# Kernel tuning notes

Hardware: AMD Instinct MI355X
Metric: run time of the kernel (lower is better)

The kernel has to match this reference:

```python
import jax, jax.numpy as jnp
import numpy as np

N_FFT = 4096
HOP = 1024
MAX_FRAMES = 345  # 44100*8 // 1024 + 1
BATCH = 8


def _build_buffers():
    N = N_FFT
    half = N // 2
    n = np.arange(N)
    k = np.arange(half + 1)
    ang = 2.0 * np.pi * np.outer(k, n) / N
    # fourier_basis = [real(fft(eye)[:half+1]); imag(fft(eye)[:half+1])], W[k,n]=exp(-2pi i kn/N)
    F = np.vstack([np.cos(ang), -np.sin(ang)])  # [N+2, N], float64
    window = 0.5 - 0.5 * np.cos(2.0 * np.pi * n / N)  # periodic hann, max == 1.0
    # rows of F are mutually orthogonal -> pinv(F) = F.T @ diag(1/||row||^2) (zero rows -> 0)
    norms = np.sum(F ** 2, axis=1)
    inv_norm = np.where(norms > 1e-6, 1.0 / norms, 0.0)
    # inverse_basis = window * pinv(F * N/HOP).T * sqrt(N)   (normalized=True)
    scale = inv_norm * (HOP / N) * np.sqrt(N)
    inverse_basis = (window[None, :] * F * scale[:, None]).astype(np.float32)  # [N+2, N]
    # window_sum normalization buffer
    T = MAX_FRAMES
    n_len = N + HOP * (T - 1)
    win_sq = (window / np.abs(window).max()) ** 2
    window_sum = np.zeros(n_len, dtype=np.float64)
    for i in range(T):
        s = i * HOP
        window_sum[s:s + N] += win_sq
    window_sum_inv = (N / (window_sum * HOP + 1e-8)).astype(np.float32)  # [n_len]
    return jnp.asarray(inverse_basis), jnp.asarray(window_sum_inv)


def setup_inputs() -> dict:
    key = jax.random.key(0)
    k1, k2 = jax.random.split(key)
    real = jax.random.normal(k1, (BATCH, N_FFT // 2 + 1, MAX_FRAMES), dtype=jnp.float32)
    imag = jax.random.normal(k2, (BATCH, N_FFT // 2 + 1, MAX_FRAMES), dtype=jnp.float32)
    inverse_basis, window_sum_inv = _build_buffers()
    return {"real": real, "imag": imag, "inverse_basis": inverse_basis,
            "window_sum_inv": window_sum_inv, "length": 352800}


def reference(real, imag, inverse_basis, window_sum_inv, length):
    eps = jnp.finfo(real.dtype).eps
    magnitude = jnp.sqrt(real ** 2 + imag ** 2)
    phase = jnp.arctan2(imag, real + eps)
    # [B, N+2, T]
    complex_input = jnp.concatenate([magnitude * jnp.cos(phase),
                                     magnitude * jnp.sin(phase)], axis=1)
    # conv_transpose1d(stride=HOP) == per-frame IDFT matmul + overlap-add
    frames = jnp.einsum('bct,ck->btk', complex_input, inverse_basis)  # [B, T, N]
    B, T, K = frames.shape
    n_len = K + HOP * (T - 1)
    idx = (jnp.arange(T)[:, None] * HOP + jnp.arange(K)[None, :]).reshape(-1)
    sig = jnp.zeros((B, n_len), frames.dtype).at[:, idx].add(frames.reshape(B, -1))
    half = K // 2
    out = sig[:, half:] * window_sum_inv[half:n_len]  # [B, n_len - half]
    if length:
        pad = max(0, length - out.shape[-1])
        out = jnp.pad(out, ((0, 0), (0, pad)))[:, :length]
    return out
```

## Files before the change

### kernel.cpp

```cpp
#include <hip/hip_runtime.h>
#include <cstdint>
#include <cstddef>

#define B_SZ  8
#define C_IN  2049
#define T_FR  345
#define NFFT  4096
#define HOPSZ 1024
#define MFR   2760
#define NPAIR 173
#define TW    1.5339807878856412e-3f

typedef float f4 __attribute__((ext_vector_type(4)));

__device__ __forceinline__ unsigned short f2b(float f) {
  union { float f; unsigned int u; } v; v.f = f;
  unsigned int r = v.u + 0x7fffu + ((v.u >> 16) & 1u);
  return (unsigned short)(r >> 16);
}
__device__ __forceinline__ float b2f(unsigned int h) {
  union { unsigned int u; float f; } v; v.u = h << 16;
  return v.f;
}

__global__ void trans(const float* __restrict__ re, const float* __restrict__ im,
                      unsigned int* __restrict__ spec) {
  __shared__ float tr[64][65];
  __shared__ float ti[64][65];
  const int tid = threadIdx.x;
  const int t0 = blockIdx.x * 64;
  const int c0 = blockIdx.y * 64;
  const int b  = blockIdx.z;
#pragma unroll
  for (int pass = 0; pass < 16; ++pass) {
    int idx = pass * 256 + tid;
    int tt = idx & 63, cc = idx >> 6;
    int c = c0 + cc, t = t0 + tt;
    float rp = 0.f, ip = 0.f;
    if (c < C_IN && t < T_FR) {
      size_t off = ((size_t)b * C_IN + c) * T_FR + t;
      float r = re[off], i = im[off];
      float x  = r + 1.1920929e-7f;
      float r2 = r * r + i * i;
      float h2 = fmaxf(x * x + i * i, 1e-35f);
      float inv = __builtin_amdgcn_sqrtf(r2) * __builtin_amdgcn_rsqf(h2);
      rp = x * inv;
      ip = i * inv;
    }
    tr[cc][tt] = rp;
    ti[cc][tt] = ip;
  }
  __syncthreads();
#pragma unroll
  for (int pass = 0; pass < 16; ++pass) {
    int idx = pass * 256 + tid;
    int kk = idx & 63, tt = idx >> 6;
    int c = c0 + kk, t = t0 + tt;
    if (c < C_IN && t < T_FR) {
      size_t mrow = (size_t)b * T_FR + t;
      unsigned int pk = ((unsigned int)f2b(ti[kk][tt]) << 16) | f2b(tr[kk][tt]);
      spec[mrow * C_IN + c] = pk;
    }
  }
}

template<int M, int L2M>
__device__ __forceinline__ void fft_stage(const f4* __restrict__ sr, const f4* __restrict__ si,
                                          f4* __restrict__ dr, f4* __restrict__ di, int tid) {
  f4 ar = sr[tid],       ai = si[tid];
  f4 br = sr[tid + 256], bi = si[tid + 256];
  f4 cr = sr[tid + 512], ci = si[tid + 512];
  f4 er = sr[tid + 768], ei = si[tid + 768];
  f4 t0r = ar + cr, t0i = ai + ci;
  f4 t1r = ar - cr, t1i = ai - ci;
  f4 t2r = br + er, t2i = bi + ei;
  f4 t3r = ei - bi, t3i = br - er;
  f4 y0r = t0r + t2r, y0i = t0i + t2i;
  f4 u1r = t1r + t3r, u1i = t1i + t3i;
  f4 u2r = t0r - t2r, u2i = t0i - t2i;
  f4 u3r = t1r - t3r, u3i = t1i - t3i;
  const int base = tid << 2;
  if (M == 1) {
#pragma unroll
    for (int p = 0; p < 4; ++p) {
      int j = base + p;
      float s1, c1; __sincosf((float)j * TW, &s1, &c1);
      float c2 = c1 * c1 - s1 * s1, s2 = 2.f * c1 * s1;
      float c3 = c2 * c1 - s2 * s1, s3 = s2 * c1 + c2 * s1;
      f4 o, oi;
      o.x  = y0r[p];
      o.y  = c1 * u1r[p] - s1 * u1i[p];
      o.z  = c2 * u2r[p] - s2 * u2i[p];
      o.w  = c3 * u3r[p] - s3 * u3i[p];
      oi.x = y0i[p];
      oi.y = c1 * u1i[p] + s1 * u1r[p];
      oi.z = c2 * u2i[p] + s2 * u2r[p];
      oi.w = c3 * u3i[p] + s3 * u3r[p];
      dr[j] = o; di[j] = oi;
    }
  } else {
    const int j  = base >> L2M;
    const int kb = (base & (M - 1)) >> 2;
    float s1, c1; __sincosf((float)(j * M) * TW, &s1, &c1);
    float c2 = c1 * c1 - s1 * s1, s2 = 2.f * c1 * s1;
    float c3 = c2 * c1 - s2 * s1, s3 = s2 * c1 + c2 * s1;
    const int wb = kb + M * j;
    const int Q  = M >> 2;
    dr[wb]         = y0r;                      di[wb]         = y0i;
    dr[wb + Q]     = c1 * u1r - s1 * u1i;      di[wb + Q]     = c1 * u1i + s1 * u1r;
    dr[wb + 2 * Q] = c2 * u2r - s2 * u2i;      di[wb + 2 * Q] = c2 * u2i + s2 * u2r;
    dr[wb + 3 * Q] = c3 * u3r - s3 * u3i;      di[wb + 3 * Q] = c3 * u3i + s3 * u3r;
  }
}

__global__ __launch_bounds__(256) void ifft_frames(const unsigned int* __restrict__ spec,
                                                   unsigned short* __restrict__ Fr) {
  __shared__ f4 B0r[1024], B0i[1024], B1r[1024], B1i[1024];
  float* r0 = (float*)B0r;
  float* i0 = (float*)B0i;
  const int tid = threadIdx.x;
  const int j = blockIdx.x, b = blockIdx.y;
  const int ta = b * T_FR + 2 * j;
  const bool hasb = (2 * j + 1) < T_FR;
  const unsigned int* spa = spec + (size_t)ta * C_IN;
  const unsigned int* spb = spa + C_IN;
#pragma unroll
  for (int p = 0; p < 8; ++p) {
    int k = p * 256 + tid;
    unsigned int va = spa[k];
    unsigned int vb = hasb ? spb[k] : 0u;
    float ar = b2f(va & 0xffffu), ai = b2f(va >> 16);
    float br = b2f(vb & 0xffffu), bi = b2f(vb >> 16);
    if (k == 0) {
      r0[0] = ar; i0[0] = br;
    } else {
      r0[k] = ar - bi;        i0[k] = ai + br;
      r0[4096 - k] = ar + bi; i0[4096 - k] = br - ai;
    }
  }
  if (tid == 0) {
    unsigned int va = spa[2048];
    unsigned int vb = hasb ? spb[2048] : 0u;
    r0[2048] = b2f(va & 0xffffu);
    i0[2048] = b2f(vb & 0xffffu);
  }
  __syncthreads();
  fft_stage<1,    0>(B0r, B0i, B1r, B1i, tid); __syncthreads();
  fft_stage<4,    2>(B1r, B1i, B0r, B0i, tid); __syncthreads();
  fft_stage<16,   4>(B0r, B0i, B1r, B1i, tid); __syncthreads();
  fft_stage<64,   6>(B1r, B1i, B0r, B0i, tid); __syncthreads();
  fft_stage<256,  8>(B0r, B0i, B1r, B1i, tid); __syncthreads();
  fft_stage<1024,10>(B1r, B1i, B0r, B0i, tid); __syncthreads();
  unsigned int* da = (unsigned int*)(Fr + (size_t)ta * NFFT);
  unsigned int* db = (unsigned int*)(Fr + (size_t)(ta + 1) * NFFT);
#pragma unroll
  for (int p = 0; p < 8; ++p) {
    int n2 = p * 256 + tid;
    int n = n2 * 2;
    float w0 = (0.5f - 0.5f * __cosf((float)n * TW)) * 0.00390625f;
    float w1 = (0.5f - 0.5f * __cosf((float)(n + 1) * TW)) * 0.00390625f;
    da[n2] = ((unsigned int)f2b(r0[n + 1] * w1) << 16) | f2b(r0[n] * w0);
    if (hasb)
      db[n2] = ((unsigned int)f2b(i0[n + 1] * w1) << 16) | f2b(i0[n] * w0);
  }
}

__global__ void ola(const unsigned short* __restrict__ Fr, const float* __restrict__ wsi,
                    float* __restrict__ out, int length) {
  int q = blockIdx.x * 256 + threadIdx.x;
  int b = blockIdx.y;
  int p4 = q * 4;
  if (p4 >= length) return;
  int s0 = (NFFT / 2) + p4;
  int tlo = (s0 - 3072) >> 10;
  tlo = tlo < 0 ? 0 : tlo;
  int thi = s0 >> 10;
  thi = thi > (T_FR - 1) ? (T_FR - 1) : thi;
  float a0 = 0.f, a1 = 0.f, a2 = 0.f, a3 = 0.f;
  for (int t = tlo; t <= thi; ++t) {
    const unsigned short* fp = Fr + ((size_t)(b * T_FR + t)) * NFFT + (s0 - (t << 10));
    ushort4 v = *(const ushort4*)fp;
    a0 += b2f(v.x); a1 += b2f(v.y); a2 += b2f(v.z); a3 += b2f(v.w);
  }
  float4 wv = *(const float4*)(wsi + s0);
  float4 o; o.x = a0 * wv.x; o.y = a1 * wv.y; o.z = a2 * wv.z; o.w = a3 * wv.w;
  *(float4*)(out + (size_t)b * length + p4) = o;
}

extern "C" void kernel_launch(void* const* d_in, const int* in_sizes, int n_in,
                              void* d_out, int out_size, void* d_ws, size_t ws_size,
                              hipStream_t stream) {
  const float* re  = (const float*)d_in[0];
  const float* im  = (const float*)d_in[1];
  const float* wsi = (const float*)d_in[3];
  float* out = (float*)d_out;
  const int length = out_size / B_SZ;

  unsigned int*   spec = (unsigned int*)d_ws;
  unsigned short* Fr   = (unsigned short*)(spec + (size_t)MFR * C_IN);

  trans<<<dim3((T_FR + 63) / 64, (C_IN + 63) / 64, B_SZ), 256, 0, stream>>>(re, im, spec);
  ifft_frames<<<dim3(NPAIR, B_SZ), 256, 0, stream>>>(spec, Fr);
  ola<<<dim3((length / 4 + 255) / 256, B_SZ), 256, 0, stream>>>(Fr, wsi, out, length);
}
```

Before: 182.7 us.

## Rewrite 4096-point IFFT as register-resident radix-16 three-pass decomposition

Replaces the six radix-4 shared-memory stages, each followed by a block barrier, with a 16x16x16 decomposition. Each thread holds 16 complex values in registers, runs a hard-coded radix-16 IDFT, and exchanges data through padded shared memory between passes. Twiddles come from a recurrence chain seeded by one sincos per pass. The output pack uses lane shuffles so even lanes write frame a and odd lanes frame b. This cuts shared-memory traffic and barriers but raises register pressure, and the chained twiddles accumulate more rounding error.

```diff
diff --git a/kernel.cpp b/kernel.cpp
--- a/kernel.cpp
+++ b/kernel.cpp
@@ -10,8 +10,11 @@
 #define MFR   2760
 #define NPAIR 173
 #define TW    1.5339807878856412e-3f
-
-typedef float f4 __attribute__((ext_vector_type(4)));
+#define TW256 2.4543692606170259e-2f
+
+#define C8P   0.70710678118654752f
+#define C16C  0.92387953251128676f
+#define C16S  0.38268343236508977f
 
 __device__ __forceinline__ unsigned short f2b(float f) {
   union { float f; unsigned int u; } v; v.f = f;
@@ -64,104 +67,138 @@
   }
 }
 
-template<int M, int L2M>
-__device__ __forceinline__ void fft_stage(const f4* __restrict__ sr, const f4* __restrict__ si,
-                                          f4* __restrict__ dr, f4* __restrict__ di, int tid) {
-  f4 ar = sr[tid],       ai = si[tid];
-  f4 br = sr[tid + 256], bi = si[tid + 256];
-  f4 cr = sr[tid + 512], ci = si[tid + 512];
-  f4 er = sr[tid + 768], ei = si[tid + 768];
-  f4 t0r = ar + cr, t0i = ai + ci;
-  f4 t1r = ar - cr, t1i = ai - ci;
-  f4 t2r = br + er, t2i = bi + ei;
-  f4 t3r = ei - bi, t3i = br - er;
-  f4 y0r = t0r + t2r, y0i = t0i + t2i;
-  f4 u1r = t1r + t3r, u1i = t1i + t3i;
-  f4 u2r = t0r - t2r, u2i = t0i - t2i;
-  f4 u3r = t1r - t3r, u3i = t1i - t3i;
-  const int base = tid << 2;
-  if (M == 1) {
-#pragma unroll
-    for (int p = 0; p < 4; ++p) {
-      int j = base + p;
-      float s1, c1; __sincosf((float)j * TW, &s1, &c1);
-      float c2 = c1 * c1 - s1 * s1, s2 = 2.f * c1 * s1;
-      float c3 = c2 * c1 - s2 * s1, s3 = s2 * c1 + c2 * s1;
-      f4 o, oi;
-      o.x  = y0r[p];
-      o.y  = c1 * u1r[p] - s1 * u1i[p];
-      o.z  = c2 * u2r[p] - s2 * u2i[p];
-      o.w  = c3 * u3r[p] - s3 * u3i[p];
-      oi.x = y0i[p];
-      oi.y = c1 * u1i[p] + s1 * u1r[p];
-      oi.z = c2 * u2i[p] + s2 * u2r[p];
-      oi.w = c3 * u3i[p] + s3 * u3r[p];
-      dr[j] = o; di[j] = oi;
-    }
-  } else {
-    const int j  = base >> L2M;
-    const int kb = (base & (M - 1)) >> 2;
-    float s1, c1; __sincosf((float)(j * M) * TW, &s1, &c1);
-    float c2 = c1 * c1 - s1 * s1, s2 = 2.f * c1 * s1;
-    float c3 = c2 * c1 - s2 * s1, s3 = s2 * c1 + c2 * s1;
-    const int wb = kb + M * j;
-    const int Q  = M >> 2;
-    dr[wb]         = y0r;                      di[wb]         = y0i;
-    dr[wb + Q]     = c1 * u1r - s1 * u1i;      di[wb + Q]     = c1 * u1i + s1 * u1r;
-    dr[wb + 2 * Q] = c2 * u2r - s2 * u2i;      di[wb + 2 * Q] = c2 * u2i + s2 * u2r;
-    dr[wb + 3 * Q] = c3 * u3r - s3 * u3i;      di[wb + 3 * Q] = c3 * u3i + s3 * u3r;
-  }
-}
-
-__global__ __launch_bounds__(256) void ifft_frames(const unsigned int* __restrict__ spec,
-                                                   unsigned short* __restrict__ Fr) {
-  __shared__ f4 B0r[1024], B0i[1024], B1r[1024], B1i[1024];
-  float* r0 = (float*)B0r;
-  float* i0 = (float*)B0i;
+__device__ __forceinline__ void cmul(float& xr, float& xi, float cr, float ci) {
+  float t = xr * cr - xi * ci;
+  xi = xr * ci + xi * cr;
+  xr = t;
+}
+
+__device__ __forceinline__ void idft16(float* zr, float* zi) {
+  float vr[16], vi[16];
+#pragma unroll
+  for (int a0 = 0; a0 < 4; ++a0) {
+    float z0r = zr[a0],      z0i = zi[a0];
+    float z1r = zr[a0 + 4],  z1i = zi[a0 + 4];
+    float z2r = zr[a0 + 8],  z2i = zi[a0 + 8];
+    float z3r = zr[a0 + 12], z3i = zi[a0 + 12];
+    float t0r = z0r + z2r, t0i = z0i + z2i;
+    float t1r = z0r - z2r, t1i = z0i - z2i;
+    float t2r = z1r + z3r, t2i = z1i + z3i;
+    float t3r = z3i - z1i, t3i = z1r - z3r;
+    vr[a0 * 4 + 0] = t0r + t2r; vi[a0 * 4 + 0] = t0i + t2i;
+    vr[a0 * 4 + 1] = t1r + t3r; vi[a0 * 4 + 1] = t1i + t3i;
+    vr[a0 * 4 + 2] = t0r - t2r; vi[a0 * 4 + 2] = t0i - t2i;
+    vr[a0 * 4 + 3] = t1r - t3r; vi[a0 * 4 + 3] = t1i - t3i;
+  }
+  cmul(vr[5],  vi[5],  C16C, C16S);
+  cmul(vr[6],  vi[6],  C8P,  C8P);
+  cmul(vr[7],  vi[7],  C16S, C16C);
+  cmul(vr[9],  vi[9],  C8P,  C8P);
+  { float t = vr[10]; vr[10] = -vi[10]; vi[10] = t; }
+  cmul(vr[11], vi[11], -C8P, C8P);
+  cmul(vr[13], vi[13], C16S, C16C);
+  cmul(vr[14], vi[14], -C8P, C8P);
+  cmul(vr[15], vi[15], -C16C, -C16S);
+#pragma unroll
+  for (int m0 = 0; m0 < 4; ++m0) {
+    float z0r = vr[0 + m0],  z0i = vi[0 + m0];
+    float z1r = vr[4 + m0],  z1i = vi[4 + m0];
+    float z2r = vr[8 + m0],  z2i = vi[8 + m0];
+    float z3r = vr[12 + m0], z3i = vi[12 + m0];
+    float t0r = z0r + z2r, t0i = z0i + z2i;
+    float t1r = z0r - z2r, t1i = z0i - z2i;
+    float t2r = z1r + z3r, t2i = z1i + z3i;
+    float t3r = z3i - z1i, t3i = z1r - z3r;
+    zr[m0 + 0]  = t0r + t2r; zi[m0 + 0]  = t0i + t2i;
+    zr[m0 + 4]  = t1r + t3r; zi[m0 + 4]  = t1i + t3i;
+    zr[m0 + 8]  = t0r - t2r; zi[m0 + 8]  = t0i - t2i;
+    zr[m0 + 12] = t1r - t3r; zi[m0 + 12] = t1i - t3i;
+  }
+}
+
+__device__ __forceinline__ void twiddle_chain(float* zr, float* zi, float step) {
+  float sA, cA; __sincosf(step, &sA, &cA);
+  float cr = cA, ci = sA;
+  cmul(zr[1], zi[1], cr, ci);
+#pragma unroll
+  for (int q = 2; q < 16; ++q) {
+    float nr = cr * cA - ci * sA;
+    ci = cr * sA + ci * cA;
+    cr = nr;
+    cmul(zr[q], zi[q], cr, ci);
+  }
+}
+
+__global__ __launch_bounds__(256, 4) void ifft_frames(const unsigned int* __restrict__ spec,
+                                                      unsigned short* __restrict__ Fr) {
+  __shared__ float LR[4352];
+  __shared__ float LI[4352];
   const int tid = threadIdx.x;
   const int j = blockIdx.x, b = blockIdx.y;
   const int ta = b * T_FR + 2 * j;
   const bool hasb = (2 * j + 1) < T_FR;
   const unsigned int* spa = spec + (size_t)ta * C_IN;
   const unsigned int* spb = spa + C_IN;
-#pragma unroll
-  for (int p = 0; p < 8; ++p) {
-    int k = p * 256 + tid;
+
+  float zr[16], zi[16];
+#pragma unroll
+  for (int q = 0; q < 16; ++q) {
+    int n = tid + 256 * q;
+    int k = (n <= 2048) ? n : (4096 - n);
     unsigned int va = spa[k];
     unsigned int vb = hasb ? spb[k] : 0u;
     float ar = b2f(va & 0xffffu), ai = b2f(va >> 16);
     float br = b2f(vb & 0xffffu), bi = b2f(vb >> 16);
-    if (k == 0) {
-      r0[0] = ar; i0[0] = br;
-    } else {
-      r0[k] = ar - bi;        i0[k] = ai + br;
-      r0[4096 - k] = ar + bi; i0[4096 - k] = br - ai;
-    }
-  }
-  if (tid == 0) {
-    unsigned int va = spa[2048];
-    unsigned int vb = hasb ? spb[2048] : 0u;
-    r0[2048] = b2f(va & 0xffffu);
-    i0[2048] = b2f(vb & 0xffffu);
-  }
-  __syncthreads();
-  fft_stage<1,    0>(B0r, B0i, B1r, B1i, tid); __syncthreads();
-  fft_stage<4,    2>(B1r, B1i, B0r, B0i, tid); __syncthreads();
-  fft_stage<16,   4>(B0r, B0i, B1r, B1i, tid); __syncthreads();
-  fft_stage<64,   6>(B1r, B1i, B0r, B0i, tid); __syncthreads();
-  fft_stage<256,  8>(B0r, B0i, B1r, B1i, tid); __syncthreads();
-  fft_stage<1024,10>(B1r, B1i, B0r, B0i, tid); __syncthreads();
+    bool dc  = (n == 0) | (n == 2048);
+    bool mir = n > 2048;
+    float zzr = mir ? (ar + bi) : (ar - bi);
+    float zzi = mir ? (br - ai) : (ai + br);
+    zr[q] = dc ? ar : zzr;
+    zi[q] = dc ? br : zzi;
+  }
+  idft16(zr, zi);
+  {
+    int base = (tid >> 4) + 17 * (tid & 15);
+#pragma unroll
+    for (int m = 0; m < 16; ++m) { LR[base + 272 * m] = zr[m]; LI[base + 272 * m] = zi[m]; }
+  }
+  __syncthreads();
+  {
+    int base = 17 * (tid & 15) + 272 * (tid >> 4);
+#pragma unroll
+    for (int q = 0; q < 16; ++q) { zr[q] = LR[base + q]; zi[q] = LI[base + q]; }
+  }
+  __syncthreads();
+  twiddle_chain(zr, zi, (float)(tid >> 4) * TW256);
+  idft16(zr, zi);
+  {
+    int base = (tid & 15) + 17 * (tid >> 4);
+#pragma unroll
+    for (int m = 0; m < 16; ++m) { LR[base + 272 * m] = zr[m]; LI[base + 272 * m] = zi[m]; }
+  }
+  __syncthreads();
+  {
+    int base = 17 * (tid & 15) + 272 * (tid >> 4);
+#pragma unroll
+    for (int q = 0; q < 16; ++q) { zr[q] = LR[base + q]; zi[q] = LI[base + q]; }
+  }
+  twiddle_chain(zr, zi, (float)tid * TW);
+  idft16(zr, zi);
   unsigned int* da = (unsigned int*)(Fr + (size_t)ta * NFFT);
   unsigned int* db = (unsigned int*)(Fr + (size_t)(ta + 1) * NFFT);
-#pragma unroll
-  for (int p = 0; p < 8; ++p) {
-    int n2 = p * 256 + tid;
-    int n = n2 * 2;
-    float w0 = (0.5f - 0.5f * __cosf((float)n * TW)) * 0.00390625f;
-    float w1 = (0.5f - 0.5f * __cosf((float)(n + 1) * TW)) * 0.00390625f;
-    da[n2] = ((unsigned int)f2b(r0[n + 1] * w1) << 16) | f2b(r0[n] * w0);
-    if (hasb)
-      db[n2] = ((unsigned int)f2b(i0[n + 1] * w1) << 16) | f2b(i0[n] * w0);
+  const bool even = (tid & 1) == 0;
+#pragma unroll
+  for (int m = 0; m < 16; ++m) {
+    int n = 256 * m + tid;
+    float w = (0.5f - 0.5f * __cosf((float)n * TW)) * 0.00390625f;
+    float va = zr[m] * w, vb = zi[m] * w;
+    float xa = __shfl_xor(va, 1);
+    float xb = __shfl_xor(vb, 1);
+    unsigned int pa = ((unsigned int)f2b(xa) << 16) | f2b(va);
+    unsigned int pb = ((unsigned int)f2b(vb) << 16) | f2b(xb);
+    int dw = 128 * m + (tid >> 1);
+    if (even)      da[dw] = pa;
+    else if (hasb) db[dw] = pb;
   }
 }
 
```

New measurement: 172.5 us. -5.6%, faster.
